# Performance work log

Hardware: AMD Instinct MI355X
Metric: run time of the kernel (lower is better)

## Reference

```python
import jax, jax.numpy as jnp
import numpy as np

SCALING = 16.0 / 16.0  # alpha / rank
TOP_K = 2


def setup_inputs() -> dict:
    key = jax.random.key(0)
    k0, k1, k2, k3, k4, k5 = jax.random.split(key, 6)
    B, N, D, O, E, R = 4, 2048, 2048, 2048, 8, 16
    x = jax.random.normal(k0, (B, N, D), jnp.float32)
    W = jax.random.normal(k1, (O, D), jnp.float32) * 0.02   # frozen base weight (out, in)
    bias = jax.random.normal(k2, (O,), jnp.float32) * 0.02
    Wr = jax.random.normal(k3, (E, D), jnp.float32) * 0.02  # router weight
    A = jax.random.normal(k4, (E, D, R), jnp.float32) * (1.0 / np.sqrt(R))
    Bexp = jax.random.normal(k5, (E, R, O), jnp.float32) * 0.01  # torch inits to zeros; random for non-trivial baseline
    return {"x": x, "W": W, "bias": bias, "Wr": Wr, "A": A, "Bexp": Bexp}


def reference(x, W, bias, Wr, A, Bexp):
    # base = F.linear(x, W, bias)
    base = jnp.einsum('bnd,od->bno', x, W) + bias
    # router logits and top-k sparse softmax weights
    logits = jnp.einsum('bnd,ed->bne', x, Wr)            # (B,N,E)
    E = logits.shape[-1]
    _, top_idx = jax.lax.top_k(logits, TOP_K)            # (B,N,K)
    keep = (jax.nn.one_hot(top_idx, E, dtype=logits.dtype).sum(axis=-2) > 0)  # (B,N,E) bool
    masked = jnp.where(keep, logits, -jnp.inf)
    router_weights = jax.nn.softmax(masked, axis=-1)     # (B,N,E)
    # MoE LoRA: sum_e w_e * (x @ A_e) @ B_e   (dropout is identity at eval/p=0)
    lora_down = jnp.einsum('bnd,edr->bner', x, A)        # (B,N,E,R)
    moe_out = jnp.einsum('bner,erd->bnd', lora_down * router_weights[..., None], Bexp)
    return base + SCALING * moe_out
```

## Files before the change

### kernel.cpp

```cpp
#include <hip/hip_runtime.h>

using f32x4  = __attribute__((ext_vector_type(4))) float;
using bf16x8 = __attribute__((ext_vector_type(8))) __bf16;

#define SB() __builtin_amdgcn_sched_barrier(0)

__device__ __forceinline__ unsigned short f2bf(float f) {
  unsigned int u = __builtin_bit_cast(unsigned int, f);
  u = (u + 0x7FFFu + ((u >> 16) & 1u)) >> 16;
  return (unsigned short)u;
}

__device__ __forceinline__ void g2lds16(const void* g, void* l) {
  __builtin_amdgcn_global_load_lds(
      (const __attribute__((address_space(1))) void*)g,
      (__attribute__((address_space(3))) void*)l, 16, 0, 0);
}

__global__ __launch_bounds__(256) void k_pre(const float* __restrict__ W,
                                             const float* __restrict__ A,
                                             const float* __restrict__ Bexp,
                                             const float* __restrict__ x,
                                             const float* __restrict__ Wr,
                                             unsigned short* __restrict__ Wb,
                                             unsigned short* __restrict__ Ab,
                                             unsigned short* __restrict__ Bb,
                                             unsigned short* __restrict__ xb,
                                             float* __restrict__ wout) {
  __shared__ float swr[8192];
  int b = blockIdx.x;
  int tid = threadIdx.x;
  if (b < 2048) {
    int wvi = tid >> 6, lane = tid & 63;
    int tok = b * 4 + wvi;
    const float4* xr = (const float4*)(x + (size_t)tok * 2048);
    float4 xv[8];
#pragma unroll
    for (int c = 0; c < 8; c++) xv[c] = xr[c * 64 + lane];
    uint2* xbw = (uint2*)(xb + (size_t)tok * 2048);
#pragma unroll
    for (int c = 0; c < 8; c++) {
      uint2 o;
      o.x = (unsigned)f2bf(xv[c].x) | ((unsigned)f2bf(xv[c].y) << 16);
      o.y = (unsigned)f2bf(xv[c].z) | ((unsigned)f2bf(xv[c].w) << 16);
      xbw[c * 64 + lane] = o;
    }
    float lg[8];
#pragma unroll
    for (int half = 0; half < 2; ++half) {
      if (half) __syncthreads();
      const float4* src = (const float4*)(Wr + half * 4 * 2048);
#pragma unroll
      for (int i = 0; i < 8; ++i) ((float4*)swr)[i * 256 + tid] = src[i * 256 + tid];
      __syncthreads();
#pragma unroll
      for (int e = 0; e < 4; ++e) {
        const float4* wv4 = (const float4*)(swr + e * 2048);
        float p = 0.f;
#pragma unroll
        for (int c = 0; c < 8; ++c) {
          float4 wv = wv4[c * 64 + lane];
          p += xv[c].x * wv.x + xv[c].y * wv.y + xv[c].z * wv.z + xv[c].w * wv.w;
        }
#pragma unroll
        for (int off = 32; off; off >>= 1) p += __shfl_xor(p, off);
        lg[half * 4 + e] = p;
      }
    }
    int i1 = 0;
#pragma unroll
    for (int e = 1; e < 8; e++) if (lg[e] > lg[i1]) i1 = e;
    int i2 = (i1 == 0) ? 1 : 0;
#pragma unroll
    for (int e = 0; e < 8; e++) { if (e == i1) continue; if (lg[e] > lg[i2]) i2 = e; }
    float e2 = expf(lg[i2] - lg[i1]);
    float den = 1.f + e2;
    if (lane < 8) wout[(size_t)tok * 8 + lane] =
        (lane == i1) ? (1.f / den) : ((lane == i2) ? (e2 / den) : 0.f);
    return;
  }
  if (b < 4096) {
    int t = (b - 2048) * 256 + tid;
    const float4* p = (const float4*)W;
    float4 a = p[2 * t], c = p[2 * t + 1];
    uint4 o;
    o.x = (unsigned)f2bf(a.x) | ((unsigned)f2bf(a.y) << 16);
    o.y = (unsigned)f2bf(a.z) | ((unsigned)f2bf(a.w) << 16);
    o.z = (unsigned)f2bf(c.x) | ((unsigned)f2bf(c.y) << 16);
    o.w = (unsigned)f2bf(c.z) | ((unsigned)f2bf(c.w) << 16);
    ((uint4*)Wb)[t] = o;
    return;
  }
  if (b < 5120) {
    int t = (b - 4096) * 256 + tid;
    int j = t >> 11, d = t & 2047;
    Ab[t] = f2bf(A[((size_t)(j >> 4) * 2048 + d) * 16 + (j & 15)]);
    return;
  }
  {
    int t = (b - 5120) * 256 + tid;
    int j = t >> 11, o = t & 2047;
    Bb[(size_t)o * 128 + j] = f2bf(Bexp[(size_t)(j >> 4) * 32768 + (j & 15) * 2048 + o]);
  }
}

__global__ __launch_bounds__(256) void k_gemm_lora(const unsigned short* __restrict__ xb,
                                                   const unsigned short* __restrict__ Ab,
                                                   const float* __restrict__ wrt,
                                                   unsigned short* __restrict__ tmat) {
  __shared__ unsigned short lds[30720];
  char* L = (char*)lds;
  const int w = threadIdx.x >> 6, lane = threadIdx.x & 63;
  const int mBase = blockIdx.y * 32;
  const int rl = lane & 15, kq = lane >> 4;
  const unsigned short* aS;
  const unsigned short* bS[4];
  {
    int r  = w * 8 + (lane >> 3);
    int cg = (lane & 7) ^ (r & 7);
    aS = xb + (size_t)(mBase + r) * 2048 + cg * 8;
  }
#pragma unroll
  for (int q = 0; q < 4; ++q) {
    int r  = (w * 4 + q) * 8 + (lane >> 3);
    int cg = (lane & 7) ^ (r & 7);
    bS[q] = Ab + (size_t)r * 2048 + cg * 8;
  }
  const int dA = w * 1024 + lane * 16;

  auto stage = [&](int tau, int buf) {
    if (tau >= 32) return;
    g2lds16(aS + tau * 64, L + buf * 4096 + dA);
#pragma unroll
    for (int q = 0; q < 4; ++q)
      g2lds16(bS[q] + tau * 64, L + 12288 + buf * 16384 + (w * 4 + q) * 1024 + lane * 16);
  };

  f32x4 z = {0.f, 0.f, 0.f, 0.f};
  f32x4 acc[2][2];
#pragma unroll
  for (int i = 0; i < 2; i++)
#pragma unroll
    for (int j = 0; j < 2; j++) acc[i][j] = z;

  stage(0, 0); stage(1, 1);
  int bR = 0, bSt = 2;

  for (int s = 0; s < 32; ++s) {
    SB();
    if (s < 31) asm volatile("s_waitcnt vmcnt(5)" ::: "memory");
    else        asm volatile("s_waitcnt vmcnt(0)" ::: "memory");
    __builtin_amdgcn_s_barrier(); SB();
    stage(s + 2, bSt);

    const char* lsA = L + bR * 4096;
    const char* lsB = L + 12288 + bR * 16384;
#pragma unroll
    for (int kk = 0; kk < 2; ++kk) {
      bf16x8 af[2], bv[2];
#pragma unroll
      for (int i = 0; i < 2; ++i) {
        int r = i * 16 + rl;
        int c = (kk * 4 + kq) ^ (r & 7);
        af[i] = *(const bf16x8*)(lsA + r * 128 + c * 16);
      }
#pragma unroll
      for (int j = 0; j < 2; ++j) {
        int r = w * 32 + j * 16 + rl;
        int c = (kk * 4 + kq) ^ (r & 7);
        bv[j] = *(const bf16x8*)(lsB + r * 128 + c * 16);
      }
#pragma unroll
      for (int i = 0; i < 2; ++i)
#pragma unroll
        for (int j = 0; j < 2; ++j)
          acc[i][j] = __builtin_amdgcn_mfma_f32_16x16x32_bf16(af[i], bv[j], acc[i][j], 0, 0, 0);
    }
    bR = (bR == 2) ? 0 : bR + 1;
    bSt = (bSt == 2) ? 0 : bSt + 1;
  }
#pragma unroll
  for (int j = 0; j < 2; ++j) {
    int jj = w * 32 + j * 16 + rl;
    int e  = jj >> 4;
#pragma unroll
    for (int i = 0; i < 2; ++i) {
      int m0 = mBase + i * 16 + kq * 4;
#pragma unroll
      for (int q = 0; q < 4; ++q) {
        int m = m0 + q;
        tmat[(size_t)m * 128 + jj] = f2bf(acc[i][j][q] * wrt[(size_t)m * 8 + e]);
      }
    }
  }
}

__global__ __launch_bounds__(256, 2) void k_gemm_main(const unsigned short* __restrict__ xb,
                                                      const unsigned short* __restrict__ Wb,
                                                      const unsigned short* __restrict__ tm,
                                                      const unsigned short* __restrict__ Bb,
                                                      const float* __restrict__ bias,
                                                      float* __restrict__ out) {
  __shared__ unsigned short lds[36864];
  char* L = (char*)lds;
  const int tid = threadIdx.x, wid = tid >> 6, lane = tid & 63;
  const int wm = wid >> 1, wn = wid & 1;
  const int bid = blockIdx.x;
  const int s = (bid & 7) * 64 + (bid >> 3);
  const int mBase = (s >> 3) * 128;
  const int nBase = (s & 7) * 256;
  const int rl = lane & 15, kq = lane >> 4;
  int aOff[4], bOff[8];
#pragma unroll
  for (int i = 0; i < 4; ++i) {
    int r = wm * 64 + i * 16 + rl;
    aOff[i] = r * 64 + ((kq ^ ((r >> 1) & 3)) << 4);
  }
#pragma unroll
  for (int j = 0; j < 8; ++j) {
    int r = wn * 128 + j * 16 + rl;
    bOff[j] = r * 64 + ((kq ^ ((r >> 1) & 3)) << 4);
  }
  const int sRo = tid >> 2;
  const int sC  = (((tid & 3) ^ ((tid >> 3) & 3)) << 3);

  const unsigned short* aSrc[2];
  const unsigned short* bSrc[4];
#pragma unroll
  for (int o = 0; o < 2; ++o) aSrc[o] = xb + (size_t)(mBase + o * 64 + sRo) * 2048 + sC;
#pragma unroll
  for (int o = 0; o < 4; ++o) bSrc[o] = Wb + (size_t)(nBase + o * 64 + sRo) * 2048 + sC;

  auto stage = [&](int tau, int bufi) {
    if (tau >= 68) return;
    if (tau < 64) {
#pragma unroll
      for (int o = 0; o < 2; ++o) {
        g2lds16(aSrc[o], L + bufi * 8192 + o * 4096 + wid * 1024);
        aSrc[o] += 32;
      }
#pragma unroll
      for (int o = 0; o < 4; ++o) {
        g2lds16(bSrc[o], L + 24576 + bufi * 16384 + o * 4096 + wid * 1024);
        bSrc[o] += 32;
      }
    } else {
      int k0 = (tau - 64) * 32;
#pragma unroll
      for (int o = 0; o < 2; ++o)
        g2lds16(tm + (size_t)(mBase + o * 64 + sRo) * 128 + k0 + sC,
                L + bufi * 8192 + o * 4096 + wid * 1024);
#pragma unroll
      for (int o = 0; o < 4; ++o)
        g2lds16(Bb + (size_t)(nBase + o * 64 + sRo) * 128 + k0 + sC,
                L + 24576 + bufi * 16384 + o * 4096 + wid * 1024);
    }
  };

  f32x4 z = {0.f, 0.f, 0.f, 0.f};
  f32x4 acc[4][8];
#pragma unroll
  for (int i = 0; i < 4; ++i)
#pragma unroll
    for (int j = 0; j < 8; ++j) acc[i][j] = z;

  stage(0, 0); stage(1, 1);
  int bR = 0, bS = 2;

  for (int t = 0; t < 68; ++t) {
    __builtin_amdgcn_sched_barrier(0);
    if (t <= 65) asm volatile("s_waitcnt vmcnt(6)" ::: "memory");
    else         asm volatile("s_waitcnt vmcnt(0)" ::: "memory");
    __builtin_amdgcn_s_barrier();
    __builtin_amdgcn_sched_barrier(0);
    stage(t + 2, bS);

    const char* bA = L + bR * 8192;
    const char* bB = L + 24576 + bR * 16384;
    bf16x8 af[4], bv[8];
#pragma unroll
    for (int j = 0; j < 8; ++j) bv[j] = *(const bf16x8*)(bB + bOff[j]);
#pragma unroll
    for (int i = 0; i < 4; ++i) af[i] = *(const bf16x8*)(bA + aOff[i]);
    __builtin_amdgcn_s_setprio(1);
#pragma unroll
    for (int i = 0; i < 4; ++i)
#pragma unroll
      for (int j = 0; j < 8; ++j)
        acc[i][j] = __builtin_amdgcn_mfma_f32_16x16x32_bf16(af[i], bv[j], acc[i][j], 0, 0, 0);
    __builtin_amdgcn_s_setprio(0);

    bR = (bR == 2) ? 0 : bR + 1;
    bS = (bS == 2) ? 0 : bS + 1;
  }

#pragma unroll
  for (int j = 0; j < 8; ++j) {
    int o = nBase + wn * 128 + j * 16 + rl;
    float bb = bias[o];
#pragma unroll
    for (int i = 0; i < 4; ++i) {
      int m0 = mBase + wm * 64 + i * 16 + kq * 4;
#pragma unroll
      for (int q = 0; q < 4; ++q)
        out[(size_t)(m0 + q) * 2048 + o] = acc[i][j][q] + bb;
    }
  }
}

extern "C" void kernel_launch(void* const* d_in, const int* in_sizes, int n_in,
                              void* d_out, int out_size, void* d_ws, size_t ws_size,
                              hipStream_t stream) {
  const float* x    = (const float*)d_in[0];
  const float* W    = (const float*)d_in[1];
  const float* bias = (const float*)d_in[2];
  const float* Wr   = (const float*)d_in[3];
  const float* A    = (const float*)d_in[4];
  const float* Bexp = (const float*)d_in[5];
  float* out = (float*)d_out;

  char* ws = (char*)d_ws;
  unsigned short* xb = (unsigned short*)(ws);
  unsigned short* Wb = (unsigned short*)(ws + 33554432);
  unsigned short* Ab = (unsigned short*)(ws + 41943040);
  unsigned short* Bb = (unsigned short*)(ws + 42467328);
  unsigned short* tm = (unsigned short*)(ws + 42991616);
  float*          wr = (float*)(ws + 45088768);

  (void)in_sizes; (void)n_in; (void)out_size; (void)ws_size;

  k_pre       <<<dim3(6144), 256, 0, stream>>>(W, A, Bexp, x, Wr, Wb, Ab, Bb, xb, wr);
  k_gemm_lora <<<dim3(1, 256), 256, 0, stream>>>(xb, Ab, wr, tm);
  k_gemm_main <<<dim3(512), 256, 0, stream>>>(xb, Wb, tm, Bb, bias, out);
}
```

Baseline: 115.1 us.

## Enlarge main GEMM tile to 256x256 with BK=64 double buffering

Reworks the main bf16 GEMM to use 256x256 output tiles per block (each wave 128x128) with a K step of 64, double-buffered in 128KB of LDS instead of a triple-buffered 128x256 tile with K step 32. A new XOR swizzle over 8 column groups matches the 128-byte rows. The larger tile raises arithmetic intensity and halves the number of barriers and K iterations. In exchange, occupancy drops to one block per CU with 256 accumulator vectors per thread, so register pressure and spills become a risk. The grid shrinks to 256 blocks, which may leave CUs idle on a 256-CU part and hurts load balance.

```diff
diff --git a/kernel.cpp b/kernel.cpp
--- a/kernel.cpp
+++ b/kernel.cpp
@@ -195,115 +195,109 @@
   }
 }
 
-__global__ __launch_bounds__(256, 2) void k_gemm_main(const unsigned short* __restrict__ xb,
+__global__ __launch_bounds__(256, 1) void k_gemm_main(const unsigned short* __restrict__ xb,
                                                       const unsigned short* __restrict__ Wb,
                                                       const unsigned short* __restrict__ tm,
                                                       const unsigned short* __restrict__ Bb,
                                                       const float* __restrict__ bias,
                                                       float* __restrict__ out) {
-  __shared__ unsigned short lds[36864];
+  __shared__ unsigned short lds[65536];
   char* L = (char*)lds;
   const int tid = threadIdx.x, wid = tid >> 6, lane = tid & 63;
   const int wm = wid >> 1, wn = wid & 1;
   const int bid = blockIdx.x;
-  const int s = (bid & 7) * 64 + (bid >> 3);
-  const int mBase = (s >> 3) * 128;
+  const int s = (bid & 7) * 32 + (bid >> 3);
+  const int mBase = (s >> 3) * 256;
   const int nBase = (s & 7) * 256;
   const int rl = lane & 15, kq = lane >> 4;
-  int aOff[4], bOff[8];
-#pragma unroll
-  for (int i = 0; i < 4; ++i) {
-    int r = wm * 64 + i * 16 + rl;
-    aOff[i] = r * 64 + ((kq ^ ((r >> 1) & 3)) << 4);
-  }
-#pragma unroll
-  for (int j = 0; j < 8; ++j) {
-    int r = wn * 128 + j * 16 + rl;
-    bOff[j] = r * 64 + ((kq ^ ((r >> 1) & 3)) << 4);
-  }
-  const int sRo = tid >> 2;
-  const int sC  = (((tid & 3) ^ ((tid >> 3) & 3)) << 3);
-
-  const unsigned short* aSrc[2];
-  const unsigned short* bSrc[4];
-#pragma unroll
-  for (int o = 0; o < 2; ++o) aSrc[o] = xb + (size_t)(mBase + o * 64 + sRo) * 2048 + sC;
-#pragma unroll
-  for (int o = 0; o < 4; ++o) bSrc[o] = Wb + (size_t)(nBase + o * 64 + sRo) * 2048 + sC;
-
-  auto stage = [&](int tau, int bufi) {
-    if (tau >= 68) return;
-    if (tau < 64) {
-#pragma unroll
-      for (int o = 0; o < 2; ++o) {
-        g2lds16(aSrc[o], L + bufi * 8192 + o * 4096 + wid * 1024);
-        aSrc[o] += 32;
-      }
-#pragma unroll
-      for (int o = 0; o < 4; ++o) {
-        g2lds16(bSrc[o], L + 24576 + bufi * 16384 + o * 4096 + wid * 1024);
-        bSrc[o] += 32;
+  const int swz0 = ((kq) ^ (rl & 7)) << 4;
+  const int swz1 = ((4 + kq) ^ (rl & 7)) << 4;
+  const int aB = (wm * 128 + rl) * 128;
+  const int bB = (wn * 128 + rl) * 128;
+  const int sr = lane >> 3;
+  const int cg = ((lane & 7) ^ sr) * 8;
+  const unsigned short* pA0 = xb + (size_t)(mBase + sr) * 2048 + cg;
+  const unsigned short* pB0 = Wb + (size_t)(nBase + sr) * 2048 + cg;
+  const unsigned short* qA0 = tm + (size_t)(mBase + sr) * 128 + cg;
+  const unsigned short* qB0 = Bb + (size_t)(nBase + sr) * 128 + cg;
+
+  auto stage = [&](int tau) {
+    if (tau >= 34) return;
+    const int d = (tau & 1) * 32768;
+    if (tau < 32) {
+      const int k0 = tau * 64;
+#pragma unroll
+      for (int o = 0; o < 8; ++o) {
+        const int rb = o * 4 + wid;
+        g2lds16(pA0 + (size_t)rb * 16384 + k0, L + d + rb * 1024);
+        g2lds16(pB0 + (size_t)rb * 16384 + k0, L + 65536 + d + rb * 1024);
       }
     } else {
-      int k0 = (tau - 64) * 32;
-#pragma unroll
-      for (int o = 0; o < 2; ++o)
-        g2lds16(tm + (size_t)(mBase + o * 64 + sRo) * 128 + k0 + sC,
-                L + bufi * 8192 + o * 4096 + wid * 1024);
-#pragma unroll
-      for (int o = 0; o < 4; ++o)
-        g2lds16(Bb + (size_t)(nBase + o * 64 + sRo) * 128 + k0 + sC,
-                L + 24576 + bufi * 16384 + o * 4096 + wid * 1024);
+      const int k0 = (tau - 32) * 64;
+#pragma unroll
+      for (int o = 0; o < 8; ++o) {
+        const int rb = o * 4 + wid;
+        g2lds16(qA0 + (size_t)rb * 1024 + k0, L + d + rb * 1024);
+        g2lds16(qB0 + (size_t)rb * 1024 + k0, L + 65536 + d + rb * 1024);
+      }
     }
   };
 
   f32x4 z = {0.f, 0.f, 0.f, 0.f};
-  f32x4 acc[4][8];
-#pragma unroll
-  for (int i = 0; i < 4; ++i)
+  f32x4 acc[8][8];
+#pragma unroll
+  for (int i = 0; i < 8; ++i)
 #pragma unroll
     for (int j = 0; j < 8; ++j) acc[i][j] = z;
 
-  stage(0, 0); stage(1, 1);
-  int bR = 0, bS = 2;
-
-  for (int t = 0; t < 68; ++t) {
-    __builtin_amdgcn_sched_barrier(0);
-    if (t <= 65) asm volatile("s_waitcnt vmcnt(6)" ::: "memory");
-    else         asm volatile("s_waitcnt vmcnt(0)" ::: "memory");
+  stage(0);
+
+  for (int t = 0; t < 34; ++t) {
+    SB();
     __builtin_amdgcn_s_barrier();
-    __builtin_amdgcn_sched_barrier(0);
-    stage(t + 2, bS);
-
-    const char* bA = L + bR * 8192;
-    const char* bB = L + 24576 + bR * 16384;
-    bf16x8 af[4], bv[8];
-#pragma unroll
-    for (int j = 0; j < 8; ++j) bv[j] = *(const bf16x8*)(bB + bOff[j]);
-#pragma unroll
-    for (int i = 0; i < 4; ++i) af[i] = *(const bf16x8*)(bA + aOff[i]);
+    SB();
+    stage(t + 1);
+    SB();
+    if (t < 33) asm volatile("s_waitcnt vmcnt(16)" ::: "memory");
+    else        asm volatile("s_waitcnt vmcnt(0)" ::: "memory");
+    SB();
+    const char* bufA = L + (t & 1) * 32768;
+    const char* bufB = L + 65536 + (t & 1) * 32768;
+    bf16x8 af[8], bv[8];
+#pragma unroll
+    for (int mi = 0; mi < 8; ++mi) af[mi] = *(const bf16x8*)(bufA + aB + mi * 2048 + swz0);
+#pragma unroll
+    for (int nj = 0; nj < 8; ++nj) bv[nj] = *(const bf16x8*)(bufB + bB + nj * 2048 + swz0);
     __builtin_amdgcn_s_setprio(1);
 #pragma unroll
-    for (int i = 0; i < 4; ++i)
-#pragma unroll
-      for (int j = 0; j < 8; ++j)
-        acc[i][j] = __builtin_amdgcn_mfma_f32_16x16x32_bf16(af[i], bv[j], acc[i][j], 0, 0, 0);
+    for (int mi = 0; mi < 8; ++mi)
+#pragma unroll
+      for (int nj = 0; nj < 8; ++nj)
+        acc[mi][nj] = __builtin_amdgcn_mfma_f32_16x16x32_bf16(af[mi], bv[nj], acc[mi][nj], 0, 0, 0);
     __builtin_amdgcn_s_setprio(0);
-
-    bR = (bR == 2) ? 0 : bR + 1;
-    bS = (bS == 2) ? 0 : bS + 1;
-  }
-
-#pragma unroll
-  for (int j = 0; j < 8; ++j) {
-    int o = nBase + wn * 128 + j * 16 + rl;
+#pragma unroll
+    for (int mi = 0; mi < 8; ++mi) af[mi] = *(const bf16x8*)(bufA + aB + mi * 2048 + swz1);
+#pragma unroll
+    for (int nj = 0; nj < 8; ++nj) bv[nj] = *(const bf16x8*)(bufB + bB + nj * 2048 + swz1);
+    __builtin_amdgcn_s_setprio(1);
+#pragma unroll
+    for (int mi = 0; mi < 8; ++mi)
+#pragma unroll
+      for (int nj = 0; nj < 8; ++nj)
+        acc[mi][nj] = __builtin_amdgcn_mfma_f32_16x16x32_bf16(af[mi], bv[nj], acc[mi][nj], 0, 0, 0);
+    __builtin_amdgcn_s_setprio(0);
+  }
+
+#pragma unroll
+  for (int nj = 0; nj < 8; ++nj) {
+    int o = nBase + wn * 128 + nj * 16 + rl;
     float bb = bias[o];
 #pragma unroll
-    for (int i = 0; i < 4; ++i) {
-      int m0 = mBase + wm * 64 + i * 16 + kq * 4;
+    for (int mi = 0; mi < 8; ++mi) {
+      int m0 = mBase + wm * 128 + mi * 16 + kq * 4;
 #pragma unroll
       for (int q = 0; q < 4; ++q)
-        out[(size_t)(m0 + q) * 2048 + o] = acc[i][j][q] + bb;
+        out[(size_t)(m0 + q) * 2048 + o] = acc[mi][nj][q] + bb;
     }
   }
 }
@@ -331,5 +325,5 @@
 
   k_pre       <<<dim3(6144), 256, 0, stream>>>(W, A, Bexp, x, Wr, Wb, Ab, Bb, xb, wr);
   k_gemm_lora <<<dim3(1, 256), 256, 0, stream>>>(xb, Ab, wr, tm);
-  k_gemm_main <<<dim3(512), 256, 0, stream>>>(xb, Wb, tm, Bb, bias, out);
-}
+  k_gemm_main <<<dim3(256), 256, 0, stream>>>(xb, Wb, tm, Bb, bias, out);
+}
```

Result: no change. 114.3 us (median of 2 runs) (-0.7%).
